# Optimization experiments

Hardware: AMD Instinct MI355X
Metric: run time of the kernel (lower is better)

Reference implementation:

```python
import jax, jax.numpy as jnp
import numpy as np

ROUTING_ITERS = 3
EPS = 1e-9


def squash(s, axis=-1):
    sq_norm = jnp.sum(s * s, axis=axis, keepdims=True)
    scale = sq_norm / (1.0 + sq_norm)
    return scale * s / jnp.sqrt(sq_norm + EPS)


def setup_inputs() -> dict:
    key = jax.random.key(0)
    k_u, k_w = jax.random.split(key)
    B, P, C, OUT, IN = 256, 2048, 10, 16, 8
    u = jax.random.normal(k_u, (B, P, IN), dtype=jnp.float32)
    W = 0.01 * jax.random.normal(k_w, (1, P, C, OUT, IN), dtype=jnp.float32)
    return {"u": u, "W": W}


def reference(u, W):
    # u: [B, P, IN], W: [1, P, C, OUT, IN]
    # u_hat[b,p,c,o] = sum_i W[0,p,c,o,i] * u[b,p,i]
    u_hat = jnp.einsum('pcoi,bpi->bpco', W[0], u)  # [B, P, C, OUT]
    B, P, C, _ = u_hat.shape
    b = jnp.zeros((B, P, C), dtype=u_hat.dtype)
    v = None
    for _ in range(ROUTING_ITERS):
        c = jax.nn.softmax(b, axis=2)                     # [B, P, C]
        s = jnp.einsum('bpc,bpco->bco', c, u_hat)         # [B, C, OUT]
        v = squash(s, axis=-1)                            # [B, C, OUT]
        b = b + jnp.einsum('bpco,bco->bpc', u_hat, v)     # agreement update
    return v
```

## Files before the change

### kernel.cpp

```cpp
#include <hip/hip_runtime.h>
#include <hip/hip_fp16.h>


#define Bn 256
#define Pn 2048
#define Cn 10
#define On 16
#define In 8
#define ROW 160
#define BT 64
#define PPB 16
#define NPT (Pn / PPB)
#define TPB 256
#define GRID ((Bn / BT) * NPT)

typedef _Float16 f16x8 __attribute__((ext_vector_type(8)));
typedef _Float16 h2f __attribute__((ext_vector_type(2)));
typedef float f32x4 __attribute__((ext_vector_type(4)));

__device__ __forceinline__ void gl_lds16(const void* g, void* l) {
  __builtin_amdgcn_global_load_lds(
      (const __attribute__((address_space(1))) unsigned int*)g,
      (__attribute__((address_space(3))) unsigned int*)l, 16, 0, 0);
}

__device__ __forceinline__ h2f pack2(float a, float b) {
  __half2 t = __floats2half2_rn(a, b);
  return *reinterpret_cast<h2f*>(&t);
}

__global__ __launch_bounds__(256) void k_prepw(const float* __restrict__ W,
                                               _Float16* __restrict__ Wh) {
  const size_t base = (size_t)blockIdx.x * 1280;
#pragma unroll
  for (int r = 0; r < 5; ++r) {
    const int i = threadIdx.x + 256 * r;
    Wh[base + i] = (_Float16)W[base + i];
  }
}

__global__ __launch_bounds__(256) void k_prepu(const float* __restrict__ u,
                                               _Float16* __restrict__ uT) {
  const int p2 = blockIdx.x * 2;
  const int b = threadIdx.x;
  const float4* src = reinterpret_cast<const float4*>(u + ((size_t)b * Pn + p2) * In);
  const float4 q0 = src[0], q1 = src[1], q2 = src[2], q3 = src[3];
  f16x8 o0, o1;
  o0[0] = (_Float16)q0.x; o0[1] = (_Float16)q0.y; o0[2] = (_Float16)q0.z; o0[3] = (_Float16)q0.w;
  o0[4] = (_Float16)q1.x; o0[5] = (_Float16)q1.y; o0[6] = (_Float16)q1.z; o0[7] = (_Float16)q1.w;
  o1[0] = (_Float16)q2.x; o1[1] = (_Float16)q2.y; o1[2] = (_Float16)q2.z; o1[3] = (_Float16)q2.w;
  o1[4] = (_Float16)q3.x; o1[5] = (_Float16)q3.y; o1[6] = (_Float16)q3.z; o1[7] = (_Float16)q3.w;
  *reinterpret_cast<f16x8*>(uT + ((size_t)p2 * Bn + b) * In) = o0;
  *reinterpret_cast<f16x8*>(uT + ((size_t)(p2 + 1) * Bn + b) * In) = o1;
}

template <int MODE>
__global__ __launch_bounds__(TPB, 2) void k_cap(const _Float16* __restrict__ uT,
                                                const _Float16* __restrict__ Wh,
                                                const float* __restrict__ s1,
                                                const float* __restrict__ s2,
                                                float* __restrict__ part) {
  __shared__ _Float16 wH[PPB * 1280];
  const int x = blockIdx.x;
  const int bt = x >> 7;
  const int pt = x & 127;
  const int tid = threadIdx.x;
  const int w = tid >> 6;
  const int lane = tid & 63;
  const int col = lane & 15;
  const int quad = lane >> 4;
  const int b = bt * BT + w * 16 + col;
  const int p0 = pt * PPB;

  {
    const char* src = reinterpret_cast<const char*>(Wh + (size_t)p0 * 1280);
    char* dst = reinterpret_cast<char*>(wH);
#pragma unroll
    for (int r = 0; r < 10; ++r)
      gl_lds16(src + r * 4096 + tid * 16, dst + r * 4096 + tid * 16);
  }

  h2f vh[Cn][2];
  if (MODE >= 1) {
    const float4* spA = reinterpret_cast<const float4*>(s1 + (size_t)b * ROW);
    const float4* spB = reinterpret_cast<const float4*>(s2 + (size_t)b * ROW);
#pragma unroll
    for (int c = 0; c < Cn; ++c) {
      const float4 a0 = spA[c * 4 + 0], a1 = spA[c * 4 + 1];
      const float4 a2 = spA[c * 4 + 2], a3 = spA[c * 4 + 3];
      float sqA = a0.x * a0.x + a0.y * a0.y + a0.z * a0.z + a0.w * a0.w;
      sqA += a1.x * a1.x + a1.y * a1.y + a1.z * a1.z + a1.w * a1.w;
      sqA += a2.x * a2.x + a2.y * a2.y + a2.z * a2.z + a2.w * a2.w;
      sqA += a3.x * a3.x + a3.y * a3.y + a3.z * a3.z + a3.w * a3.w;
      sqA *= 0.01f;
      const float facA = 0.1f * (sqA / (1.f + sqA)) / sqrtf(sqA + 1e-9f);
      const float4 qa = spA[c * 4 + quad];
      float v0 = facA * qa.x, v1_ = facA * qa.y;
      float v2_ = facA * qa.z, v3_ = facA * qa.w;
      if (MODE == 2) {
        const float4 b0 = spB[c * 4 + 0], b1 = spB[c * 4 + 1];
        const float4 b2 = spB[c * 4 + 2], b3 = spB[c * 4 + 3];
        float sqB = b0.x * b0.x + b0.y * b0.y + b0.z * b0.z + b0.w * b0.w;
        sqB += b1.x * b1.x + b1.y * b1.y + b1.z * b1.z + b1.w * b1.w;
        sqB += b2.x * b2.x + b2.y * b2.y + b2.z * b2.z + b2.w * b2.w;
        sqB += b3.x * b3.x + b3.y * b3.y + b3.z * b3.z + b3.w * b3.w;
        const float facB = (sqB / (1.f + sqB)) / sqrtf(sqB + 1e-9f);
        const float4 qb = spB[c * 4 + quad];
        v0 += facB * qb.x; v1_ += facB * qb.y;
        v2_ += facB * qb.z; v3_ += facB * qb.w;
      }
      vh[c][0] = pack2(v0, v1_);
      vh[c][1] = pack2(v2_, v3_);
    }
  }

  f32x4 acc[Cn];
  const f32x4 zc = {0.f, 0.f, 0.f, 0.f};
#pragma unroll
  for (int c = 0; c < Cn; ++c) acc[c] = zc;

  const _Float16* urow = uT + ((size_t)p0 * Bn + b) * In;
  f16x8 ufA = *reinterpret_cast<const f16x8*>(urow);
  f16x8 ufB = *reinterpret_cast<const f16x8*>(urow + (size_t)Bn * In);
  const f16x8 zb = {0, 0, 0, 0, 0, 0, 0, 0};
  const bool isq0 = (quad == 0);

  __syncthreads();

  for (int ip = 0; ip < PPB; ip += 2) {
    f16x8 nfA = ufA, nfB = ufB;
    if (ip + 2 < PPB) {
      nfA = *reinterpret_cast<const f16x8*>(urow + (size_t)(ip + 2) * Bn * In);
      nfB = *reinterpret_cast<const f16x8*>(urow + (size_t)(ip + 3) * Bn * In);
    }
    const f16x8 ubA = isq0 ? ufA : zb;
    const f16x8 ubB = isq0 ? ufB : zb;
    const _Float16* wpA = wH + (size_t)ip * 1280 + col * 8;
    const _Float16* wpB = wpA + 1280;

    if (MODE == 0) {
#pragma unroll
      for (int c = 0; c < Cn; ++c) {
        const f16x8 aWA = *reinterpret_cast<const f16x8*>(wpA + c * 128);
        const f16x8 aWB = *reinterpret_cast<const f16x8*>(wpB + c * 128);
        acc[c] = __builtin_amdgcn_mfma_f32_16x16x32_f16(aWA, ubA, acc[c], 0, 0, 0);
        acc[c] = __builtin_amdgcn_mfma_f32_16x16x32_f16(aWB, ubB, acc[c], 0, 0, 0);
      }
    } else {
      float lfA[Cn], lfB[Cn];
      h2f uhA[Cn][2], uhB[Cn][2];
#pragma unroll
      for (int c = 0; c < Cn; ++c) {
        const f16x8 aWA = *reinterpret_cast<const f16x8*>(wpA + c * 128);
        const f16x8 aWB = *reinterpret_cast<const f16x8*>(wpB + c * 128);
        const f32x4 dA =
            __builtin_amdgcn_mfma_f32_16x16x32_f16(aWA, ubA, zc, 0, 0, 0);
        const f32x4 dB =
            __builtin_amdgcn_mfma_f32_16x16x32_f16(aWB, ubB, zc, 0, 0, 0);
        float la = dA[0] * (float)vh[c][0][0];
        la = __builtin_fmaf(dA[1], (float)vh[c][0][1], la);
        la = __builtin_fmaf(dA[2], (float)vh[c][1][0], la);
        la = __builtin_fmaf(dA[3], (float)vh[c][1][1], la);
        lfA[c] = la;
        float lb = dB[0] * (float)vh[c][0][0];
        lb = __builtin_fmaf(dB[1], (float)vh[c][0][1], lb);
        lb = __builtin_fmaf(dB[2], (float)vh[c][1][0], lb);
        lb = __builtin_fmaf(dB[3], (float)vh[c][1][1], lb);
        lfB[c] = lb;
        uhA[c][0] = pack2(dA[0], dA[1]);
        uhA[c][1] = pack2(dA[2], dA[3]);
        uhB[c][0] = pack2(dB[0], dB[1]);
        uhB[c][1] = pack2(dB[2], dB[3]);
      }
#pragma unroll
      for (int c = 0; c < Cn; ++c) {
        lfA[c] += __shfl_xor(lfA[c], 16, 64);
        lfB[c] += __shfl_xor(lfB[c], 16, 64);
        lfA[c] += __shfl_xor(lfA[c], 32, 64);
        lfB[c] += __shfl_xor(lfB[c], 32, 64);
      }
      float mA = fmaxf(fmaxf(lfA[0], lfA[1]), fmaxf(lfA[2], lfA[3]));
      float mB = fmaxf(fmaxf(lfB[0], lfB[1]), fmaxf(lfB[2], lfB[3]));
      mA = fmaxf(mA, fmaxf(fmaxf(lfA[4], lfA[5]), fmaxf(lfA[6], lfA[7])));
      mB = fmaxf(mB, fmaxf(fmaxf(lfB[4], lfB[5]), fmaxf(lfB[6], lfB[7])));
      mA = fmaxf(mA, fmaxf(lfA[8], lfA[9]));
      mB = fmaxf(mB, fmaxf(lfB[8], lfB[9]));
      float ssA = 0.f, ssB = 0.f;
#pragma unroll
      for (int c = 0; c < Cn; ++c) {
        lfA[c] = __expf(lfA[c] - mA);
        ssA += lfA[c];
        lfB[c] = __expf(lfB[c] - mB);
        ssB += lfB[c];
      }
      const float invA = 1.f / ssA;
      const float invB = 1.f / ssB;
#pragma unroll
      for (int c = 0; c < Cn; ++c) {
        const float cvA = lfA[c] * invA;
        const float cvB = lfB[c] * invB;
        float t0 = __builtin_fmaf(cvA, (float)uhA[c][0][0], acc[c][0]);
        float t1 = __builtin_fmaf(cvA, (float)uhA[c][0][1], acc[c][1]);
        float t2 = __builtin_fmaf(cvA, (float)uhA[c][1][0], acc[c][2]);
        float t3 = __builtin_fmaf(cvA, (float)uhA[c][1][1], acc[c][3]);
        acc[c][0] = __builtin_fmaf(cvB, (float)uhB[c][0][0], t0);
        acc[c][1] = __builtin_fmaf(cvB, (float)uhB[c][0][1], t1);
        acc[c][2] = __builtin_fmaf(cvB, (float)uhB[c][1][0], t2);
        acc[c][3] = __builtin_fmaf(cvB, (float)uhB[c][1][1], t3);
      }
    }
    ufA = nfA;
    ufB = nfB;
  }

  float* pb = part + ((size_t)x * BT + w * 16 + col) * ROW;
#pragma unroll
  for (int c = 0; c < Cn; ++c)
    *reinterpret_cast<f32x4*>(pb + c * 16 + quad * 4) = acc[c];
}

__global__ __launch_bounds__(256) void k_red(const float* __restrict__ part,
                                             float* __restrict__ s) {
  const int cell = blockIdx.x * 256 + threadIdx.x;
  const int chunk = blockIdx.y;
  const int b = cell / 160, rem = cell - 160 * b;
  const int bt = b >> 6, bl = b & 63;
  const float* p0 =
      part + ((size_t)(bt * NPT + chunk * 32) * BT + bl) * ROW + rem;
  float a0 = 0.f, a1 = 0.f, a2 = 0.f, a3 = 0.f;
  float a4 = 0.f, a5 = 0.f, a6 = 0.f, a7 = 0.f;
#pragma unroll
  for (int pt = 0; pt < 32; pt += 8) {
    a0 += p0[(size_t)(pt + 0) * BT * ROW];
    a1 += p0[(size_t)(pt + 1) * BT * ROW];
    a2 += p0[(size_t)(pt + 2) * BT * ROW];
    a3 += p0[(size_t)(pt + 3) * BT * ROW];
    a4 += p0[(size_t)(pt + 4) * BT * ROW];
    a5 += p0[(size_t)(pt + 5) * BT * ROW];
    a6 += p0[(size_t)(pt + 6) * BT * ROW];
    a7 += p0[(size_t)(pt + 7) * BT * ROW];
  }
  atomicAdd(&s[cell], ((a0 + a1) + (a2 + a3)) + ((a4 + a5) + (a6 + a7)));
}

__global__ __launch_bounds__(256) void k_out(const float* __restrict__ s,
                                             float* __restrict__ out) {
  const int gi = blockIdx.x * 256 + threadIdx.x;
  const int b = gi / 10, c = gi - 10 * b;
  const float* sp = s + (size_t)b * ROW + c * 16;
  float sq = 0.f;
#pragma unroll
  for (int o = 0; o < On; ++o) { const float xx = sp[o]; sq += xx * xx; }
  const float fac = (sq / (1.f + sq)) / sqrtf(sq + 1e-9f);
  float* op = out + (size_t)b * ROW + c * 16;
#pragma unroll
  for (int o = 0; o < On; ++o) op[o] = fac * sp[o];
}

extern "C" void kernel_launch(void* const* d_in, const int* in_sizes, int n_in,
                              void* d_out, int out_size, void* d_ws, size_t ws_size,
                              hipStream_t stream) {
  (void)in_sizes; (void)n_in; (void)out_size;
  const float* u = (const float*)d_in[0];
  const float* W = (const float*)d_in[1];
  float* out = (float*)d_out;
  float* s1 = (float*)d_ws;
  float* s2 = s1 + (size_t)Bn * ROW;
  float* s3 = s2 + (size_t)Bn * ROW;
  float* part = s3 + (size_t)Bn * ROW;
  _Float16* Wh = (_Float16*)(part + (size_t)GRID * BT * ROW);
  _Float16* uTp = Wh + (size_t)Pn * Cn * On * In;
  const size_t need =
      ((size_t)3 * Bn * ROW + (size_t)GRID * BT * ROW) * sizeof(float) +
      ((size_t)Pn * Cn * On * In + (size_t)Pn * Bn * In) * sizeof(_Float16);
  if (ws_size < need) return;
  hipMemsetAsync(s1, 0, (size_t)3 * Bn * ROW * sizeof(float), stream);
  k_prepw<<<Pn, 256, 0, stream>>>(W, Wh);
  k_prepu<<<Pn / 2, 256, 0, stream>>>(u, uTp);
  k_cap<0><<<GRID, TPB, 0, stream>>>(uTp, Wh, s1, s1, part);
  k_red<<<dim3(160, 4), 256, 0, stream>>>(part, s1);
  k_cap<1><<<GRID, TPB, 0, stream>>>(uTp, Wh, s1, s1, part);
  k_red<<<dim3(160, 4), 256, 0, stream>>>(part, s2);
  k_cap<2><<<GRID, TPB, 0, stream>>>(uTp, Wh, s1, s2, part);
  k_red<<<dim3(160, 4), 256, 0, stream>>>(part, s3);
  k_out<<<10, 256, 0, stream>>>(s3, out);
}
```

Measured before the change: 184.4 us.

## Split the point loop across two wave groups with an LDS partial-sum reduction

The capsule kernel block grows to 512 threads. Two groups of four waves each handle half of the block's 16 points, so each thread's serial MFMA/routing loop is half as long and more waves are available to hide latency. The W staging loop is adjusted to 512 threads. The two groups' accumulators are combined through an LDS arena reused from the W buffer, which adds two barriers and an LDS round trip. The stronger launch-bounds occupancy request may constrain registers, and the 162-float row stride leaves the 16-byte LDS accesses only 8-byte aligned.

```diff
diff --git a/kernel.cpp b/kernel.cpp
--- a/kernel.cpp
+++ b/kernel.cpp
@@ -11,7 +11,7 @@
 #define BT 64
 #define PPB 16
 #define NPT (Pn / PPB)
-#define TPB 256
+#define TPB 512
 #define GRID ((Bn / BT) * NPT)
 
 typedef _Float16 f16x8 __attribute__((ext_vector_type(8)));
@@ -55,29 +55,32 @@
 }
 
 template <int MODE>
-__global__ __launch_bounds__(TPB, 2) void k_cap(const _Float16* __restrict__ uT,
+__global__ __launch_bounds__(TPB, 4) void k_cap(const _Float16* __restrict__ uT,
                                                 const _Float16* __restrict__ Wh,
                                                 const float* __restrict__ s1,
                                                 const float* __restrict__ s2,
                                                 float* __restrict__ part) {
-  __shared__ _Float16 wH[PPB * 1280];
+  __shared__ float arena[10368];
+  _Float16* wH = reinterpret_cast<_Float16*>(arena);
   const int x = blockIdx.x;
   const int bt = x >> 7;
   const int pt = x & 127;
   const int tid = threadIdx.x;
   const int w = tid >> 6;
+  const int pg = w >> 2;
+  const int wq = w & 3;
   const int lane = tid & 63;
   const int col = lane & 15;
   const int quad = lane >> 4;
-  const int b = bt * BT + w * 16 + col;
+  const int b = bt * BT + wq * 16 + col;
   const int p0 = pt * PPB;
 
   {
     const char* src = reinterpret_cast<const char*>(Wh + (size_t)p0 * 1280);
     char* dst = reinterpret_cast<char*>(wH);
 #pragma unroll
-    for (int r = 0; r < 10; ++r)
-      gl_lds16(src + r * 4096 + tid * 16, dst + r * 4096 + tid * 16);
+    for (int r = 0; r < 5; ++r)
+      gl_lds16(src + r * 8192 + tid * 16, dst + r * 8192 + tid * 16);
   }
 
   h2f vh[Cn][2];
@@ -119,7 +122,7 @@
 #pragma unroll
   for (int c = 0; c < Cn; ++c) acc[c] = zc;
 
-  const _Float16* urow = uT + ((size_t)p0 * Bn + b) * In;
+  const _Float16* urow = uT + ((size_t)(p0 + pg * 8) * Bn + b) * In;
   f16x8 ufA = *reinterpret_cast<const f16x8*>(urow);
   f16x8 ufB = *reinterpret_cast<const f16x8*>(urow + (size_t)Bn * In);
   const f16x8 zb = {0, 0, 0, 0, 0, 0, 0, 0};
@@ -127,15 +130,15 @@
 
   __syncthreads();
 
-  for (int ip = 0; ip < PPB; ip += 2) {
+  for (int ip = 0; ip < 8; ip += 2) {
     f16x8 nfA = ufA, nfB = ufB;
-    if (ip + 2 < PPB) {
+    if (ip + 2 < 8) {
       nfA = *reinterpret_cast<const f16x8*>(urow + (size_t)(ip + 2) * Bn * In);
       nfB = *reinterpret_cast<const f16x8*>(urow + (size_t)(ip + 3) * Bn * In);
     }
     const f16x8 ubA = isq0 ? ufA : zb;
     const f16x8 ubB = isq0 ? ufB : zb;
-    const _Float16* wpA = wH + (size_t)ip * 1280 + col * 8;
+    const _Float16* wpA = wH + (size_t)(pg * 8 + ip) * 1280 + col * 8;
     const _Float16* wpB = wpA + 1280;
 
     if (MODE == 0) {
@@ -213,10 +216,26 @@
     ufB = nfB;
   }
 
-  float* pb = part + ((size_t)x * BT + w * 16 + col) * ROW;
-#pragma unroll
-  for (int c = 0; c < Cn; ++c)
-    *reinterpret_cast<f32x4*>(pb + c * 16 + quad * 4) = acc[c];
+  __syncthreads();
+  float* sAcc = arena;
+  const int row = wq * 16 + col;
+  if (pg == 1) {
+    float* dst = &sAcc[row * 162 + quad * 4];
+#pragma unroll
+    for (int c = 0; c < Cn; ++c)
+      *reinterpret_cast<f32x4*>(dst + c * 16) = acc[c];
+  }
+  __syncthreads();
+  if (pg == 0) {
+    const float* srcp = &sAcc[row * 162 + quad * 4];
+    float* pb = part + ((size_t)x * BT + row) * ROW;
+#pragma unroll
+    for (int c = 0; c < Cn; ++c) {
+      f32x4 t = *reinterpret_cast<const f32x4*>(srcp + c * 16);
+      t = t + acc[c];
+      *reinterpret_cast<f32x4*>(pb + c * 16 + quad * 4) = t;
+    }
+  }
 }
 
 __global__ __launch_bounds__(256) void k_red(const float* __restrict__ part,
```

New measurement: 401.5 us. +117.7%, slower.
